# Performance work log

Hardware: AMD Instinct MI355X
Metric: run time of the kernel (lower is better)

## Reference

```python
import jax, jax.numpy as jnp
import numpy as np

D_MODEL = 512
N_HEADS = 8
D_K = D_MODEL // N_HEADS
D_FF = 2048
N = 4096
EPS = 1e-5


def _layer_norm(x, g, b):
    mu = jnp.mean(x, axis=-1, keepdims=True)
    var = jnp.mean(jnp.square(x - mu), axis=-1, keepdims=True)
    return (x - mu) * jax.lax.rsqrt(var + EPS) * g + b


def setup_inputs() -> dict:
    key = jax.random.key(0)
    ks = jax.random.split(key, 16)
    s = 1.0 / np.sqrt(D_MODEL)
    sf = 1.0 / np.sqrt(D_FF)
    inp = {
        "h": jax.random.normal(ks[0], (N, D_MODEL), dtype=jnp.float32),
        "adj": jax.random.randint(ks[1], (N, N), 0, 2, dtype=jnp.int32),
        "Wq": jax.random.uniform(ks[2], (D_MODEL, D_MODEL), jnp.float32, -s, s),
        "bq": jnp.zeros((D_MODEL,), jnp.float32),
        "Wk": jax.random.uniform(ks[3], (D_MODEL, D_MODEL), jnp.float32, -s, s),
        "bk": jnp.zeros((D_MODEL,), jnp.float32),
        "Wv": jax.random.uniform(ks[4], (D_MODEL, D_MODEL), jnp.float32, -s, s),
        "bv": jnp.zeros((D_MODEL,), jnp.float32),
        "Wo": jax.random.uniform(ks[5], (D_MODEL, D_MODEL), jnp.float32, -s, s),
        "bo": jnp.zeros((D_MODEL,), jnp.float32),
        "W1": jax.random.uniform(ks[6], (D_FF, D_MODEL), jnp.float32, -s, s),
        "b1": jnp.zeros((D_FF,), jnp.float32),
        "W2": jax.random.uniform(ks[7], (D_MODEL, D_FF), jnp.float32, -sf, sf),
        "b2": jnp.zeros((D_MODEL,), jnp.float32),
        "ln1_g": jnp.ones((D_MODEL,), jnp.float32),
        "ln1_b": jnp.zeros((D_MODEL,), jnp.float32),
        "ln2_g": jnp.ones((D_MODEL,), jnp.float32),
        "ln2_b": jnp.zeros((D_MODEL,), jnp.float32),
    }
    return inp


def reference(h, adj, Wq, bq, Wk, bk, Wv, bv, Wo, bo, W1, b1, W2, b2,
              ln1_g, ln1_b, ln2_g, ln2_b):
    n = h.shape[0]
    # adjacency + self loops, used as attention mask (batch=1)
    mask = adj.astype(jnp.float32) + jnp.eye(n, dtype=jnp.float32)  # [N,N]

    # QKV projections, split into heads: [N, H, Dk]
    q = (h @ Wq.T + bq).reshape(n, N_HEADS, D_K)
    k = (h @ Wk.T + bk).reshape(n, N_HEADS, D_K)
    v = (h @ Wv.T + bv).reshape(n, N_HEADS, D_K)

    scores = jnp.einsum("nhd,mhd->hnm", q, k) / jnp.sqrt(jnp.float32(D_K))
    scores = jnp.where(mask[None, :, :] == 0, jnp.float32(-1e9), scores)
    attn = jax.nn.softmax(scores, axis=-1)  # dropout is identity in eval
    ctx = jnp.einsum("hnm,mhd->nhd", attn, v).reshape(n, D_MODEL)
    attn_out = ctx @ Wo.T + bo

    h1 = _layer_norm(h + attn_out, ln1_g, ln1_b)
    ff = jax.nn.relu(h1 @ W1.T + b1) @ W2.T + b2
    h2 = _layer_norm(h1 + ff, ln2_g, ln2_b)
    return h2
```

## Files before the change

### kernel.cpp

```cpp
#include <hip/hip_runtime.h>
#include <stdint.h>
#include <stddef.h>

typedef __bf16 bf16;
typedef __bf16 bf16x8 __attribute__((ext_vector_type(8)));
typedef float  f32x4  __attribute__((ext_vector_type(4)));

struct CastArgs {
  const float* src[17];
  bf16*        dst[17];
  int          cum[18];
};

__global__ __launch_bounds__(256) void k_cast(CastArgs a, int total8)
{
  const int g = blockIdx.x * 256 + threadIdx.x;
  if (g >= total8) return;
  int t = 0;
  while (a.cum[t + 1] <= g) ++t;
  const int i = g - a.cum[t];
  const float4* s = (const float4*)(a.src[t]) + (size_t)i * 2;
  const float4 x0 = s[0], x1 = s[1];
  bf16x8 y;
  y[0] = (bf16)x0.x; y[1] = (bf16)x0.y; y[2] = (bf16)x0.z; y[3] = (bf16)x0.w;
  y[4] = (bf16)x1.x; y[5] = (bf16)x1.y; y[6] = (bf16)x1.z; y[7] = (bf16)x1.w;
  *(bf16x8*)(a.dst[t] + (size_t)i * 8) = y;
}

__device__ __forceinline__ void gemm_tile_128(
    const bf16* __restrict__ A, const bf16* __restrict__ B,
    const bf16* __restrict__ bias, bf16* __restrict__ C,
    int N, int K, int m0, int n0, int relu)
{
  __shared__ __align__(16) bf16 As[128 * 72];
  __shared__ __align__(16) bf16 Bs[128 * 72];

  const int tid    = threadIdx.x;
  const int lane   = tid & 63;
  const int wave   = tid >> 6;
  const int lane15 = lane & 15;
  const int quad   = lane >> 4;
  const int wm     = (wave & 1) << 6;
  const int wn     = (wave >> 1) << 6;

  f32x4 acc[4][4] = {};

  const bf16* Ab = A + (size_t)m0 * K;
  const bf16* Bb = B + (size_t)n0 * K;

  for (int k0 = 0; k0 < K; k0 += 64) {
    bf16x8 ar[4], br[4];
#pragma unroll
    for (int i = 0; i < 4; ++i) {
      const int c = i * 256 + tid;
      const int row = c >> 3, col = (c & 7) * 8;
      ar[i] = *(const bf16x8*)&Ab[(size_t)row * K + k0 + col];
      br[i] = *(const bf16x8*)&Bb[(size_t)row * K + k0 + col];
    }
    __syncthreads();
#pragma unroll
    for (int i = 0; i < 4; ++i) {
      const int c = i * 256 + tid;
      const int row = c >> 3, col = c & 7;
      *(bf16x8*)&As[row * 72 + col * 8] = ar[i];
      *(bf16x8*)&Bs[row * 72 + col * 8] = br[i];
    }
    __syncthreads();

#pragma unroll
    for (int kk = 0; kk < 2; ++kk) {
      bf16x8 af[4], bfr[4];
#pragma unroll
      for (int f = 0; f < 4; ++f) {
        const int ra = wm + f * 16 + lane15;
        af[f]  = *(const bf16x8*)&As[ra * 72 + (kk * 4 + quad) * 8];
        const int rb = wn + f * 16 + lane15;
        bfr[f] = *(const bf16x8*)&Bs[rb * 72 + (kk * 4 + quad) * 8];
      }
#pragma unroll
      for (int fm = 0; fm < 4; ++fm)
#pragma unroll
        for (int fn = 0; fn < 4; ++fn)
          acc[fm][fn] = __builtin_amdgcn_mfma_f32_16x16x32_bf16(
              af[fm], bfr[fn], acc[fm][fn], 0, 0, 0);
    }
  }

#pragma unroll
  for (int fm = 0; fm < 4; ++fm) {
#pragma unroll
    for (int fn = 0; fn < 4; ++fn) {
      const int col = n0 + wn + fn * 16 + lane15;
      const float bv = (float)bias[col];
#pragma unroll
      for (int r = 0; r < 4; ++r) {
        const int row = m0 + wm + fm * 16 + quad * 4 + r;
        float v = acc[fm][fn][r] + bv;
        if (relu) v = fmaxf(v, 0.0f);
        C[(size_t)row * N + col] = (bf16)v;
      }
    }
  }
}

__global__ __launch_bounds__(256, 2) void k_gemm(
    const bf16* __restrict__ A, const bf16* __restrict__ B,
    const bf16* __restrict__ bias, bf16* __restrict__ C,
    int N, int K, int relu)
{
  gemm_tile_128(A, B, bias, C, N, K, blockIdx.x * 128, blockIdx.y * 128, relu);
}

__global__ __launch_bounds__(256, 2) void k_gemm_qkv(
    const bf16* __restrict__ h,
    const bf16* __restrict__ Wq, const bf16* __restrict__ Wk, const bf16* __restrict__ Wv,
    const bf16* __restrict__ bq, const bf16* __restrict__ bk, const bf16* __restrict__ bv,
    bf16* __restrict__ q, bf16* __restrict__ k, bf16* __restrict__ v,
    int N, int K)
{
  const bf16* B; const bf16* bias; bf16* C;
  if (blockIdx.z == 0)      { B = Wq; bias = bq; C = q; }
  else if (blockIdx.z == 1) { B = Wk; bias = bk; C = k; }
  else                      { B = Wv; bias = bv; C = v; }
  gemm_tile_128(h, B, bias, C, N, K, blockIdx.x * 128, blockIdx.y * 128, 0);
}

__global__ __launch_bounds__(256, 2) void k_gemm_sk(
    const bf16* __restrict__ A, const bf16* __restrict__ B,
    float* __restrict__ Cp, int N, int K, int Ksplit)
{
  __shared__ __align__(16) bf16 As[128 * 72];
  __shared__ __align__(16) bf16 Bs[128 * 72];

  const int tid    = threadIdx.x;
  const int lane   = tid & 63;
  const int wave   = tid >> 6;
  const int lane15 = lane & 15;
  const int quad   = lane >> 4;
  const int wm     = (wave & 1) << 6;
  const int wn     = (wave >> 1) << 6;
  const int m0     = blockIdx.x * 128;
  const int n0     = blockIdx.y * 128;
  const int kbeg   = blockIdx.z * Ksplit;

  f32x4 acc[4][4] = {};

  const bf16* Ab = A + (size_t)m0 * K;
  const bf16* Bb = B + (size_t)n0 * K;

  for (int k0 = kbeg; k0 < kbeg + Ksplit; k0 += 64) {
    bf16x8 ar[4], br[4];
#pragma unroll
    for (int i = 0; i < 4; ++i) {
      const int c = i * 256 + tid;
      const int row = c >> 3, col = (c & 7) * 8;
      ar[i] = *(const bf16x8*)&Ab[(size_t)row * K + k0 + col];
      br[i] = *(const bf16x8*)&Bb[(size_t)row * K + k0 + col];
    }
    __syncthreads();
#pragma unroll
    for (int i = 0; i < 4; ++i) {
      const int c = i * 256 + tid;
      const int row = c >> 3, col = c & 7;
      *(bf16x8*)&As[row * 72 + col * 8] = ar[i];
      *(bf16x8*)&Bs[row * 72 + col * 8] = br[i];
    }
    __syncthreads();

#pragma unroll
    for (int kk = 0; kk < 2; ++kk) {
      bf16x8 af[4], bfr[4];
#pragma unroll
      for (int f = 0; f < 4; ++f) {
        const int ra = wm + f * 16 + lane15;
        af[f]  = *(const bf16x8*)&As[ra * 72 + (kk * 4 + quad) * 8];
        const int rb = wn + f * 16 + lane15;
        bfr[f] = *(const bf16x8*)&Bs[rb * 72 + (kk * 4 + quad) * 8];
      }
#pragma unroll
      for (int fm = 0; fm < 4; ++fm)
#pragma unroll
        for (int fn = 0; fn < 4; ++fn)
          acc[fm][fn] = __builtin_amdgcn_mfma_f32_16x16x32_bf16(
              af[fm], bfr[fn], acc[fm][fn], 0, 0, 0);
    }
  }

  float* Cz = Cp + (size_t)blockIdx.z * 4096 * N;
#pragma unroll
  for (int fm = 0; fm < 4; ++fm)
#pragma unroll
    for (int fn = 0; fn < 4; ++fn) {
      const int col = n0 + wn + fn * 16 + lane15;
#pragma unroll
      for (int r = 0; r < 4; ++r) {
        const int row = m0 + wm + fm * 16 + quad * 4 + r;
        Cz[(size_t)row * N + col] = acc[fm][fn][r];
      }
    }
}

__global__ __launch_bounds__(256) void k_sk_combine(
    const float* __restrict__ Cp, const bf16* __restrict__ bias,
    bf16* __restrict__ C, int N)
{
  const int g = blockIdx.x * 256 + threadIdx.x;
  const size_t base = (size_t)g * 8;
  const int col = (int)(base % (size_t)N);
  const float* p0 = Cp + base;
  const float* p1 = Cp + (size_t)4096 * N + base;
  f32x4 a0 = *(const f32x4*)p0, a1 = *(const f32x4*)(p0 + 4);
  f32x4 b0 = *(const f32x4*)p1, b1 = *(const f32x4*)(p1 + 4);
  bf16x8 y;
#pragma unroll
  for (int j = 0; j < 4; ++j) {
    y[j]     = (bf16)(a0[j] + b0[j] + (float)bias[col + j]);
    y[4 + j] = (bf16)(a1[j] + b1[j] + (float)bias[col + 4 + j]);
  }
  *(bf16x8*)(C + base) = y;
}

__global__ __launch_bounds__(256) void k_packmask(
    const int* __restrict__ adj, unsigned long long* __restrict__ mb)
{
  const int gw   = (int)((blockIdx.x * 256 + threadIdx.x) >> 6);
  const int lane = threadIdx.x & 63;
  const int a    = adj[(size_t)gw * 64 + lane];
  unsigned long long m = __ballot(a != 0);
  const int row = gw >> 6, wc = gw & 63;
  if ((row >> 6) == wc) m |= 1ull << (row & 63);
  if (lane == 0) mb[gw] = m;
}

__global__ __launch_bounds__(256) void k_transpose_v(
    const bf16* __restrict__ v, bf16* __restrict__ vt)
{
  __shared__ __align__(16) bf16 T[64 * 72];
  const int r0 = blockIdx.x * 64;
  const int c0 = blockIdx.y * 64;
  const int tid = threadIdx.x;
#pragma unroll
  for (int rr = 0; rr < 2; ++rr) {
    int idx = rr * 256 + tid;
    int kr = idx >> 3, ch = (idx & 7) * 8;
    *(bf16x8*)&T[kr * 72 + ch] = *(const bf16x8*)&v[(size_t)(r0 + kr) * 512 + c0 + ch];
  }
  __syncthreads();
#pragma unroll
  for (int rr = 0; rr < 2; ++rr) {
    int idx = rr * 256 + tid;
    int cr = idx >> 3, ch = idx & 7;
    bf16x8 y;
#pragma unroll
    for (int j = 0; j < 8; ++j) y[j] = T[(ch * 8 + j) * 72 + cr];
    *(bf16x8*)&vt[(size_t)(c0 + cr) * 4096 + r0 + ch * 8] = y;
  }
}

__global__ __launch_bounds__(256, 4) void k_attn(
    const bf16* __restrict__ Q, const bf16* __restrict__ Km,
    const bf16* __restrict__ Vt, const unsigned long long* __restrict__ mb,
    bf16* __restrict__ Opart, float* __restrict__ Lpart)
{
  __shared__ __align__(16) bf16 Ks[64 * 72];
  __shared__ __align__(16) bf16 Vs[64 * 72];
  __shared__ __align__(16) bf16 Plb[4][16 * 72];

  const int tid    = threadIdx.x;
  const int wave   = tid >> 6;
  const int lane   = tid & 63;
  const int lane15 = lane & 15;
  const int quad   = lane >> 4;
  const int sp     = blockIdx.x & 3;
  const int hd     = (blockIdx.x >> 2) & 7;
  const int qt     = blockIdx.x >> 5;
  const int qrow   = qt * 64 + wave * 16;

  bf16x8 qf[2];
#pragma unroll
  for (int c = 0; c < 2; ++c)
    qf[c] = *(const bf16x8*)&Q[(size_t)(qrow + lane15) * 512 + hd * 64 + c * 32 + quad * 8];

  bf16x8 ones;
#pragma unroll
  for (int j = 0; j < 8; ++j) ones[j] = (bf16)1.0f;

  f32x4 o[4] = {};
  f32x4 la   = {};

  for (int kt = sp * 16; kt < sp * 16 + 16; ++kt) {
    const int kb = kt * 64;
#pragma unroll
    for (int rr = 0; rr < 2; ++rr) {
      int idx = rr * 256 + tid;
      int a = idx >> 3, ch = (idx & 7) * 8;
      *(bf16x8*)&Ks[a * 72 + ch] = *(const bf16x8*)&Km[(size_t)(kb + a) * 512 + hd * 64 + ch];
      *(bf16x8*)&Vs[a * 72 + ch] = *(const bf16x8*)&Vt[(size_t)(hd * 64 + a) * 4096 + kb + ch];
    }
    __syncthreads();

    unsigned long long mw[4];
#pragma unroll
    for (int r = 0; r < 4; ++r)
      mw[r] = mb[(size_t)(qrow + quad * 4 + r) * 64 + kt] >> lane15;

#pragma unroll
    for (int g = 0; g < 4; ++g) {
      bf16x8 k0f = *(const bf16x8*)&Ks[(g * 16 + lane15) * 72 + quad * 8];
      bf16x8 k1f = *(const bf16x8*)&Ks[(g * 16 + lane15) * 72 + 32 + quad * 8];
      f32x4 s = {};
      s = __builtin_amdgcn_mfma_f32_16x16x32_bf16(qf[0], k0f, s, 0, 0, 0);
      s = __builtin_amdgcn_mfma_f32_16x16x32_bf16(qf[1], k1f, s, 0, 0, 0);
#pragma unroll
      for (int r = 0; r < 4; ++r) {
        const bool ok = ((mw[r] >> (g * 16)) & 1ull) != 0;
        const float p = ok ? __expf(s[r] * 0.125f) : 0.0f;
        Plb[wave][(quad * 4 + r) * 72 + g * 16 + lane15] = (bf16)p;
      }
    }

#pragma unroll
    for (int c2 = 0; c2 < 2; ++c2) {
      bf16x8 pa = *(const bf16x8*)&Plb[wave][lane15 * 72 + c2 * 32 + quad * 8];
      la = __builtin_amdgcn_mfma_f32_16x16x32_bf16(pa, ones, la, 0, 0, 0);
#pragma unroll
      for (int g2 = 0; g2 < 4; ++g2) {
        bf16x8 vf = *(const bf16x8*)&Vs[(g2 * 16 + lane15) * 72 + c2 * 32 + quad * 8];
        o[g2] = __builtin_amdgcn_mfma_f32_16x16x32_bf16(pa, vf, o[g2], 0, 0, 0);
      }
    }
    __syncthreads();
  }

  bf16* Oz = Opart + (size_t)sp * 4096 * 512;
#pragma unroll
  for (int g2 = 0; g2 < 4; ++g2)
#pragma unroll
    for (int r = 0; r < 4; ++r) {
      const int row = qrow + quad * 4 + r;
      Oz[(size_t)row * 512 + hd * 64 + g2 * 16 + lane15] = (bf16)o[g2][r];
    }
  if (lane15 == 0) {
#pragma unroll
    for (int r = 0; r < 4; ++r)
      Lpart[sp * 32768 + (qrow + quad * 4 + r) * 8 + hd] = la[r];
  }
}

__global__ __launch_bounds__(256) void k_attn_combine(
    const bf16* __restrict__ Opart, const float* __restrict__ Lpart,
    bf16* __restrict__ ctx)
{
  const int g = blockIdx.x * 256 + threadIdx.x;
  const size_t base = (size_t)g * 8;
  const int row = g >> 6;
  const int hd  = (g & 63) >> 3;
  float acc[8] = {};
  float l = 0.0f;
#pragma unroll
  for (int s = 0; s < 4; ++s) {
    bf16x8 ov = *(const bf16x8*)&Opart[(size_t)s * 4096 * 512 + base];
#pragma unroll
    for (int j = 0; j < 8; ++j) acc[j] += (float)ov[j];
    l += Lpart[s * 32768 + row * 8 + hd];
  }
  const float rl = 1.0f / l;
  bf16x8 y;
#pragma unroll
  for (int j = 0; j < 8; ++j) y[j] = (bf16)(acc[j] * rl);
  *(bf16x8*)(ctx + base) = y;
}

template <int F32OUT>
__global__ __launch_bounds__(256) void k_addln(
    const bf16* __restrict__ x, const bf16* __restrict__ y,
    const bf16* __restrict__ gam, const bf16* __restrict__ bet,
    void* __restrict__ out)
{
  const int wave = threadIdx.x >> 6, lane = threadIdx.x & 63;
  const int row  = blockIdx.x * 4 + wave;
  const size_t base = (size_t)row * 512 + lane * 8;
  bf16x8 xv = *(const bf16x8*)(x + base);
  bf16x8 yv = *(const bf16x8*)(y + base);
  float v[8], s = 0.0f, s2 = 0.0f;
#pragma unroll
  for (int j = 0; j < 8; ++j) {
    v[j] = (float)xv[j] + (float)yv[j];
    s += v[j]; s2 += v[j] * v[j];
  }
#pragma unroll
  for (int d = 1; d < 64; d <<= 1) { s += __shfl_xor(s, d, 64); s2 += __shfl_xor(s2, d, 64); }
  const float mu  = s * (1.0f / 512.0f);
  const float var = s2 * (1.0f / 512.0f) - mu * mu;
  const float rs  = rsqrtf(var + 1e-5f);
  bf16x8 gv = *(const bf16x8*)(gam + lane * 8);
  bf16x8 bv = *(const bf16x8*)(bet + lane * 8);
  if (F32OUT) {
    float* o = (float*)out + base;
#pragma unroll
    for (int j = 0; j < 8; ++j)
      o[j] = ((v[j] - mu) * rs) * (float)gv[j] + (float)bv[j];
  } else {
    bf16x8 ov;
#pragma unroll
    for (int j = 0; j < 8; ++j)
      ov[j] = (bf16)(((v[j] - mu) * rs) * (float)gv[j] + (float)bv[j]);
    *(bf16x8*)((bf16*)out + base) = ov;
  }
}

extern "C" void kernel_launch(void* const* d_in, const int* in_sizes, int n_in,
                              void* d_out, int out_size, void* d_ws, size_t ws_size,
                              hipStream_t stream)
{
  const int* adj = (const int*)d_in[1];

  char* ws = (char*)d_ws;
  const size_t MB = 1024 * 1024;

  bf16* hb  = (bf16*)(ws + 0 * MB);
  bf16* Wqb = (bf16*)(ws + 4 * MB);
  bf16* Wkb = (bf16*)(ws + 4 * MB + 512 * 1024);
  bf16* Wvb = (bf16*)(ws + 5 * MB);
  bf16* Wob = (bf16*)(ws + 5 * MB + 512 * 1024);
  bf16* W1b = (bf16*)(ws + 6 * MB);
  bf16* W2b = (bf16*)(ws + 8 * MB);
  char* vecbase = ws + 10 * MB;
  bf16* bqb  = (bf16*)(vecbase + 0 * 16384);
  bf16* bkb  = (bf16*)(vecbase + 1 * 16384);
  bf16* bvb  = (bf16*)(vecbase + 2 * 16384);
  bf16* bob  = (bf16*)(vecbase + 3 * 16384);
  bf16* b1b  = (bf16*)(vecbase + 4 * 16384);
  bf16* b2b  = (bf16*)(vecbase + 5 * 16384);
  bf16* g1b  = (bf16*)(vecbase + 6 * 16384);
  bf16* be1b = (bf16*)(vecbase + 7 * 16384);
  bf16* g2b  = (bf16*)(vecbase + 8 * 16384);
  bf16* be2b = (bf16*)(vecbase + 9 * 16384);

  bf16* q    = (bf16*)(ws + 12 * MB);
  bf16* k    = (bf16*)(ws + 16 * MB);
  bf16* v    = (bf16*)(ws + 20 * MB);
  bf16* vt   = (bf16*)(ws + 24 * MB);
  unsigned long long* mbits = (unsigned long long*)(ws + 28 * MB);
  bf16* ctx  = (bf16*)(ws + 30 * MB);
  bf16*  Opart = (bf16*)(ws + 34 * MB);
  float* Lpart = (float*)(ws + 50 * MB);
  float* skP  = (float*)(ws + 34 * MB);
  bf16* att  = (bf16*)(ws + 12 * MB);
  bf16* h1   = (bf16*)(ws + 30 * MB);
  bf16* ff1  = (bf16*)(ws + 12 * MB);
  bf16* ff2  = (bf16*)(ws + 12 * MB);

  CastArgs ca;
  const int srcIdx[17] = {0, 2, 3, 4, 5, 6, 7, 8, 9, 10, 11, 12, 13, 14, 15, 16, 17};
  bf16* dsts[17] = {hb, Wqb, bqb, Wkb, bkb, Wvb, bvb, Wob, bob,
                    W1b, b1b, W2b, b2b, g1b, be1b, g2b, be2b};
  int cum = 0;
  for (int t = 0; t < 17; ++t) {
    ca.src[t] = (const float*)d_in[srcIdx[t]];
    ca.dst[t] = dsts[t];
    ca.cum[t] = cum;
    cum += in_sizes[srcIdx[t]] / 8;
  }
  ca.cum[17] = cum;

  const dim3 blk(256);
  k_cast<<<dim3((cum + 255) / 256), blk, 0, stream>>>(ca, cum);

  k_gemm_qkv<<<dim3(32, 4, 3), blk, 0, stream>>>(hb, Wqb, Wkb, Wvb, bqb, bkb, bvb,
                                                 q, k, v, 512, 512);
  k_transpose_v<<<dim3(64, 8), blk, 0, stream>>>(v, vt);
  k_packmask<<<dim3(65536), blk, 0, stream>>>(adj, mbits);
  k_attn<<<dim3(2048), blk, 0, stream>>>(q, k, vt, mbits, Opart, Lpart);
  k_attn_combine<<<dim3(1024), blk, 0, stream>>>(Opart, Lpart, ctx);
  k_gemm_sk<<<dim3(32, 4, 2), blk, 0, stream>>>(ctx, Wob, skP, 512, 512, 256);
  k_sk_combine<<<dim3(1024), blk, 0, stream>>>(skP, bob, att, 512);
  k_addln<0><<<dim3(1024), blk, 0, stream>>>(hb, att, g1b, be1b, (void*)h1);
  k_gemm<<<dim3(32, 16), blk, 0, stream>>>(h1, W1b, b1b, ff1, 2048, 512, 1);
  k_gemm_sk<<<dim3(32, 4, 2), blk, 0, stream>>>(ff1, W2b, skP, 512, 2048, 1024);
  k_sk_combine<<<dim3(1024), blk, 0, stream>>>(skP, b2b, ff2, 512);
  k_addln<1><<<dim3(1024), blk, 0, stream>>>(h1, ff2, g2b, be2b, d_out);
}
```

Baseline: 322.3 us.

## Async LDS GEMM loads, fuse split-K combine into LayerNorm, widen attention tiles

GEMM tiles now use global_load_lds async copies into an XOR-swizzled unpadded LDS layout instead of register staging. The split-K combine kernels are folded into the add+LayerNorm kernels, which removes two launches and an intermediate round trip through memory. The attention kernel processes 32 query rows per wave, halving the grid and reusing K/V fragments across two M tiles. Bias and LayerNorm vectors are read directly as fp32, so they no longer go through the cast kernel. The wider attention tiles raise register and LDS pressure, and the async path adds a trailing barrier each k-step.

```diff
diff --git a/kernel.cpp b/kernel.cpp
--- a/kernel.cpp
+++ b/kernel.cpp
@@ -6,10 +6,18 @@
 typedef __bf16 bf16x8 __attribute__((ext_vector_type(8)));
 typedef float  f32x4  __attribute__((ext_vector_type(4)));
 
+typedef __attribute__((address_space(3))) void       lds_void;
+typedef __attribute__((address_space(1))) const void gbl_cvoid;
+
+#define ASYNC_CP16(g, l) \
+  __builtin_amdgcn_global_load_lds((gbl_cvoid*)(g), (lds_void*)(l), 16, 0, 0)
+
+__device__ __forceinline__ int swz(int r) { return (r & 7) ^ ((r & 8) >> 1); }
+
 struct CastArgs {
-  const float* src[17];
-  bf16*        dst[17];
-  int          cum[18];
+  const float* src[7];
+  bf16*        dst[7];
+  int          cum[8];
 };
 
 __global__ __launch_bounds__(256) void k_cast(CastArgs a, int total8)
@@ -27,14 +35,11 @@
   *(bf16x8*)(a.dst[t] + (size_t)i * 8) = y;
 }
 
-__device__ __forceinline__ void gemm_tile_128(
+__device__ __forceinline__ void gemm_core_async(
     const bf16* __restrict__ A, const bf16* __restrict__ B,
-    const bf16* __restrict__ bias, bf16* __restrict__ C,
-    int N, int K, int m0, int n0, int relu)
-{
-  __shared__ __align__(16) bf16 As[128 * 72];
-  __shared__ __align__(16) bf16 Bs[128 * 72];
-
+    bf16* As, bf16* Bs, f32x4 (&acc)[4][4],
+    int K, int m0, int n0, int kbeg, int kend)
+{
   const int tid    = threadIdx.x;
   const int lane   = tid & 63;
   const int wave   = tid >> 6;
@@ -43,27 +48,22 @@
   const int wm     = (wave & 1) << 6;
   const int wn     = (wave >> 1) << 6;
 
-  f32x4 acc[4][4] = {};
+  int srow[4], soff[4];
+#pragma unroll
+  for (int i = 0; i < 4; ++i) {
+    int c   = ((wave * 4 + i) << 6) + lane;
+    srow[i] = c >> 3;
+    soff[i] = ((c & 7) ^ swz(srow[i])) * 8;
+  }
 
   const bf16* Ab = A + (size_t)m0 * K;
   const bf16* Bb = B + (size_t)n0 * K;
 
-  for (int k0 = 0; k0 < K; k0 += 64) {
-    bf16x8 ar[4], br[4];
+  for (int k0 = kbeg; k0 < kend; k0 += 64) {
 #pragma unroll
     for (int i = 0; i < 4; ++i) {
-      const int c = i * 256 + tid;
-      const int row = c >> 3, col = (c & 7) * 8;
-      ar[i] = *(const bf16x8*)&Ab[(size_t)row * K + k0 + col];
-      br[i] = *(const bf16x8*)&Bb[(size_t)row * K + k0 + col];
-    }
-    __syncthreads();
-#pragma unroll
-    for (int i = 0; i < 4; ++i) {
-      const int c = i * 256 + tid;
-      const int row = c >> 3, col = c & 7;
-      *(bf16x8*)&As[row * 72 + col * 8] = ar[i];
-      *(bf16x8*)&Bs[row * 72 + col * 8] = br[i];
+      ASYNC_CP16(Ab + (size_t)srow[i] * K + k0 + soff[i], &As[(wave * 4 + i) * 512]);
+      ASYNC_CP16(Bb + (size_t)srow[i] * K + k0 + soff[i], &Bs[(wave * 4 + i) * 512]);
     }
     __syncthreads();
 
@@ -73,9 +73,9 @@
 #pragma unroll
       for (int f = 0; f < 4; ++f) {
         const int ra = wm + f * 16 + lane15;
-        af[f]  = *(const bf16x8*)&As[ra * 72 + (kk * 4 + quad) * 8];
+        af[f]  = *(const bf16x8*)&As[ra * 64 + (((kk * 4 + quad) ^ swz(ra)) * 8)];
         const int rb = wn + f * 16 + lane15;
-        bfr[f] = *(const bf16x8*)&Bs[rb * 72 + (kk * 4 + quad) * 8];
+        bfr[f] = *(const bf16x8*)&Bs[rb * 64 + (((kk * 4 + quad) ^ swz(rb)) * 8)];
       }
 #pragma unroll
       for (int fm = 0; fm < 4; ++fm)
@@ -84,14 +84,31 @@
           acc[fm][fn] = __builtin_amdgcn_mfma_f32_16x16x32_bf16(
               af[fm], bfr[fn], acc[fm][fn], 0, 0, 0);
     }
-  }
-
-#pragma unroll
-  for (int fm = 0; fm < 4; ++fm) {
+    __syncthreads();
+  }
+}
+
+__global__ __launch_bounds__(256, 2) void k_gemm(
+    const bf16* __restrict__ A, const bf16* __restrict__ B,
+    const float* __restrict__ bias, bf16* __restrict__ C,
+    int N, int K, int relu)
+{
+  __shared__ __align__(16) bf16 As[128 * 64];
+  __shared__ __align__(16) bf16 Bs[128 * 64];
+  const int m0 = blockIdx.x * 128, n0 = blockIdx.y * 128;
+  f32x4 acc[4][4] = {};
+  gemm_core_async(A, B, As, Bs, acc, K, m0, n0, 0, K);
+
+  const int lane15 = threadIdx.x & 15;
+  const int quad   = (threadIdx.x & 63) >> 4;
+  const int wave   = threadIdx.x >> 6;
+  const int wm     = (wave & 1) << 6, wn = (wave >> 1) << 6;
+#pragma unroll
+  for (int fm = 0; fm < 4; ++fm)
 #pragma unroll
     for (int fn = 0; fn < 4; ++fn) {
       const int col = n0 + wn + fn * 16 + lane15;
-      const float bv = (float)bias[col];
+      const float bv = bias[col];
 #pragma unroll
       for (int r = 0; r < 4; ++r) {
         const int row = m0 + wm + fm * 16 + quad * 4 + r;
@@ -100,92 +117,57 @@
         C[(size_t)row * N + col] = (bf16)v;
       }
     }
-  }
-}
-
-__global__ __launch_bounds__(256, 2) void k_gemm(
-    const bf16* __restrict__ A, const bf16* __restrict__ B,
-    const bf16* __restrict__ bias, bf16* __restrict__ C,
-    int N, int K, int relu)
-{
-  gemm_tile_128(A, B, bias, C, N, K, blockIdx.x * 128, blockIdx.y * 128, relu);
 }
 
 __global__ __launch_bounds__(256, 2) void k_gemm_qkv(
     const bf16* __restrict__ h,
     const bf16* __restrict__ Wq, const bf16* __restrict__ Wk, const bf16* __restrict__ Wv,
-    const bf16* __restrict__ bq, const bf16* __restrict__ bk, const bf16* __restrict__ bv,
-    bf16* __restrict__ q, bf16* __restrict__ k, bf16* __restrict__ v,
-    int N, int K)
-{
-  const bf16* B; const bf16* bias; bf16* C;
+    const float* __restrict__ bq, const float* __restrict__ bk, const float* __restrict__ bv,
+    bf16* __restrict__ q, bf16* __restrict__ k, bf16* __restrict__ v)
+{
+  __shared__ __align__(16) bf16 As[128 * 64];
+  __shared__ __align__(16) bf16 Bs[128 * 64];
+  const bf16* B; const float* bias; bf16* C;
   if (blockIdx.z == 0)      { B = Wq; bias = bq; C = q; }
   else if (blockIdx.z == 1) { B = Wk; bias = bk; C = k; }
   else                      { B = Wv; bias = bv; C = v; }
-  gemm_tile_128(h, B, bias, C, N, K, blockIdx.x * 128, blockIdx.y * 128, 0);
+  const int m0 = blockIdx.x * 128, n0 = blockIdx.y * 128;
+  f32x4 acc[4][4] = {};
+  gemm_core_async(h, B, As, Bs, acc, 512, m0, n0, 0, 512);
+
+  const int lane15 = threadIdx.x & 15;
+  const int quad   = (threadIdx.x & 63) >> 4;
+  const int wave   = threadIdx.x >> 6;
+  const int wm     = (wave & 1) << 6, wn = (wave >> 1) << 6;
+#pragma unroll
+  for (int fm = 0; fm < 4; ++fm)
+#pragma unroll
+    for (int fn = 0; fn < 4; ++fn) {
+      const int col = n0 + wn + fn * 16 + lane15;
+      const float bv = bias[col];
+#pragma unroll
+      for (int r = 0; r < 4; ++r) {
+        const int row = m0 + wm + fm * 16 + quad * 4 + r;
+        C[(size_t)row * 512 + col] = (bf16)(acc[fm][fn][r] + bv);
+      }
+    }
 }
 
 __global__ __launch_bounds__(256, 2) void k_gemm_sk(
     const bf16* __restrict__ A, const bf16* __restrict__ B,
     float* __restrict__ Cp, int N, int K, int Ksplit)
 {
-  __shared__ __align__(16) bf16 As[128 * 72];
-  __shared__ __align__(16) bf16 Bs[128 * 72];
-
-  const int tid    = threadIdx.x;
-  const int lane   = tid & 63;
-  const int wave   = tid >> 6;
-  const int lane15 = lane & 15;
-  const int quad   = lane >> 4;
-  const int wm     = (wave & 1) << 6;
-  const int wn     = (wave >> 1) << 6;
-  const int m0     = blockIdx.x * 128;
-  const int n0     = blockIdx.y * 128;
-  const int kbeg   = blockIdx.z * Ksplit;
-
+  __shared__ __align__(16) bf16 As[128 * 64];
+  __shared__ __align__(16) bf16 Bs[128 * 64];
+  const int m0 = blockIdx.x * 128, n0 = blockIdx.y * 128;
+  const int kbeg = blockIdx.z * Ksplit;
   f32x4 acc[4][4] = {};
-
-  const bf16* Ab = A + (size_t)m0 * K;
-  const bf16* Bb = B + (size_t)n0 * K;
-
-  for (int k0 = kbeg; k0 < kbeg + Ksplit; k0 += 64) {
-    bf16x8 ar[4], br[4];
-#pragma unroll
-    for (int i = 0; i < 4; ++i) {
-      const int c = i * 256 + tid;
-      const int row = c >> 3, col = (c & 7) * 8;
-      ar[i] = *(const bf16x8*)&Ab[(size_t)row * K + k0 + col];
-      br[i] = *(const bf16x8*)&Bb[(size_t)row * K + k0 + col];
-    }
-    __syncthreads();
-#pragma unroll
-    for (int i = 0; i < 4; ++i) {
-      const int c = i * 256 + tid;
-      const int row = c >> 3, col = c & 7;
-      *(bf16x8*)&As[row * 72 + col * 8] = ar[i];
-      *(bf16x8*)&Bs[row * 72 + col * 8] = br[i];
-    }
-    __syncthreads();
-
-#pragma unroll
-    for (int kk = 0; kk < 2; ++kk) {
-      bf16x8 af[4], bfr[4];
-#pragma unroll
-      for (int f = 0; f < 4; ++f) {
-        const int ra = wm + f * 16 + lane15;
-        af[f]  = *(const bf16x8*)&As[ra * 72 + (kk * 4 + quad) * 8];
-        const int rb = wn + f * 16 + lane15;
-        bfr[f] = *(const bf16x8*)&Bs[rb * 72 + (kk * 4 + quad) * 8];
-      }
-#pragma unroll
-      for (int fm = 0; fm < 4; ++fm)
-#pragma unroll
-        for (int fn = 0; fn < 4; ++fn)
-          acc[fm][fn] = __builtin_amdgcn_mfma_f32_16x16x32_bf16(
-              af[fm], bfr[fn], acc[fm][fn], 0, 0, 0);
-    }
-  }
-
+  gemm_core_async(A, B, As, Bs, acc, K, m0, n0, kbeg, kbeg + Ksplit);
+
+  const int lane15 = threadIdx.x & 15;
+  const int quad   = (threadIdx.x & 63) >> 4;
+  const int wave   = threadIdx.x >> 6;
+  const int wm     = (wave & 1) << 6, wn = (wave >> 1) << 6;
   float* Cz = Cp + (size_t)blockIdx.z * 4096 * N;
 #pragma unroll
   for (int fm = 0; fm < 4; ++fm)
@@ -198,26 +180,6 @@
         Cz[(size_t)row * N + col] = acc[fm][fn][r];
       }
     }
-}
-
-__global__ __launch_bounds__(256) void k_sk_combine(
-    const float* __restrict__ Cp, const bf16* __restrict__ bias,
-    bf16* __restrict__ C, int N)
-{
-  const int g = blockIdx.x * 256 + threadIdx.x;
-  const size_t base = (size_t)g * 8;
-  const int col = (int)(base % (size_t)N);
-  const float* p0 = Cp + base;
-  const float* p1 = Cp + (size_t)4096 * N + base;
-  f32x4 a0 = *(const f32x4*)p0, a1 = *(const f32x4*)(p0 + 4);
-  f32x4 b0 = *(const f32x4*)p1, b1 = *(const f32x4*)(p1 + 4);
-  bf16x8 y;
-#pragma unroll
-  for (int j = 0; j < 4; ++j) {
-    y[j]     = (bf16)(a0[j] + b0[j] + (float)bias[col + j]);
-    y[4 + j] = (bf16)(a1[j] + b1[j] + (float)bias[col + 4 + j]);
-  }
-  *(bf16x8*)(C + base) = y;
 }
 
 __global__ __launch_bounds__(256) void k_packmask(
@@ -264,7 +226,7 @@
 {
   __shared__ __align__(16) bf16 Ks[64 * 72];
   __shared__ __align__(16) bf16 Vs[64 * 72];
-  __shared__ __align__(16) bf16 Plb[4][16 * 72];
+  __shared__ __align__(16) bf16 Plb[4][32 * 72];
 
   const int tid    = threadIdx.x;
   const int wave   = tid >> 6;
@@ -274,19 +236,22 @@
   const int sp     = blockIdx.x & 3;
   const int hd     = (blockIdx.x >> 2) & 7;
   const int qt     = blockIdx.x >> 5;
-  const int qrow   = qt * 64 + wave * 16;
-
-  bf16x8 qf[2];
-#pragma unroll
-  for (int c = 0; c < 2; ++c)
-    qf[c] = *(const bf16x8*)&Q[(size_t)(qrow + lane15) * 512 + hd * 64 + c * 32 + quad * 8];
+  const int qrow   = qt * 128 + wave * 32;
+
+  bf16x8 qf[2][2];
+#pragma unroll
+  for (int mt = 0; mt < 2; ++mt)
+#pragma unroll
+    for (int c = 0; c < 2; ++c)
+      qf[mt][c] = *(const bf16x8*)&Q[(size_t)(qrow + mt * 16 + lane15) * 512 +
+                                     hd * 64 + c * 32 + quad * 8];
 
   bf16x8 ones;
 #pragma unroll
   for (int j = 0; j < 8; ++j) ones[j] = (bf16)1.0f;
 
-  f32x4 o[4] = {};
-  f32x4 la   = {};
+  f32x4 o[2][4] = {};
+  f32x4 la[2]   = {};
 
   for (int kt = sp * 16; kt < sp * 16 + 16; ++kt) {
     const int kb = kt * 64;
@@ -299,51 +264,64 @@
     }
     __syncthreads();
 
-    unsigned long long mw[4];
-#pragma unroll
-    for (int r = 0; r < 4; ++r)
-      mw[r] = mb[(size_t)(qrow + quad * 4 + r) * 64 + kt] >> lane15;
+    unsigned long long mw[2][4];
+#pragma unroll
+    for (int mt = 0; mt < 2; ++mt)
+#pragma unroll
+      for (int r = 0; r < 4; ++r)
+        mw[mt][r] = mb[(size_t)(qrow + mt * 16 + quad * 4 + r) * 64 + kt] >> lane15;
 
 #pragma unroll
     for (int g = 0; g < 4; ++g) {
       bf16x8 k0f = *(const bf16x8*)&Ks[(g * 16 + lane15) * 72 + quad * 8];
       bf16x8 k1f = *(const bf16x8*)&Ks[(g * 16 + lane15) * 72 + 32 + quad * 8];
-      f32x4 s = {};
-      s = __builtin_amdgcn_mfma_f32_16x16x32_bf16(qf[0], k0f, s, 0, 0, 0);
-      s = __builtin_amdgcn_mfma_f32_16x16x32_bf16(qf[1], k1f, s, 0, 0, 0);
+#pragma unroll
+      for (int mt = 0; mt < 2; ++mt) {
+        f32x4 s = {};
+        s = __builtin_amdgcn_mfma_f32_16x16x32_bf16(qf[mt][0], k0f, s, 0, 0, 0);
+        s = __builtin_amdgcn_mfma_f32_16x16x32_bf16(qf[mt][1], k1f, s, 0, 0, 0);
+#pragma unroll
+        for (int r = 0; r < 4; ++r) {
+          const bool ok = ((mw[mt][r] >> (g * 16)) & 1ull) != 0;
+          const float p = ok ? __expf(s[r] * 0.125f) : 0.0f;
+          Plb[wave][(mt * 16 + quad * 4 + r) * 72 + g * 16 + lane15] = (bf16)p;
+        }
+      }
+    }
+
+#pragma unroll
+    for (int c2 = 0; c2 < 2; ++c2) {
+      bf16x8 vf[4];
+#pragma unroll
+      for (int g2 = 0; g2 < 4; ++g2)
+        vf[g2] = *(const bf16x8*)&Vs[(g2 * 16 + lane15) * 72 + c2 * 32 + quad * 8];
+#pragma unroll
+      for (int mt = 0; mt < 2; ++mt) {
+        bf16x8 pa = *(const bf16x8*)&Plb[wave][(mt * 16 + lane15) * 72 + c2 * 32 + quad * 8];
+        la[mt] = __builtin_amdgcn_mfma_f32_16x16x32_bf16(pa, ones, la[mt], 0, 0, 0);
+#pragma unroll
+        for (int g2 = 0; g2 < 4; ++g2)
+          o[mt][g2] = __builtin_amdgcn_mfma_f32_16x16x32_bf16(pa, vf[g2], o[mt][g2], 0, 0, 0);
+      }
+    }
+    __syncthreads();
+  }
+
+  bf16* Oz = Opart + (size_t)sp * 4096 * 512;
+#pragma unroll
+  for (int mt = 0; mt < 2; ++mt) {
+#pragma unroll
+    for (int g2 = 0; g2 < 4; ++g2)
 #pragma unroll
       for (int r = 0; r < 4; ++r) {
-        const bool ok = ((mw[r] >> (g * 16)) & 1ull) != 0;
-        const float p = ok ? __expf(s[r] * 0.125f) : 0.0f;
-        Plb[wave][(quad * 4 + r) * 72 + g * 16 + lane15] = (bf16)p;
-      }
-    }
-
-#pragma unroll
-    for (int c2 = 0; c2 < 2; ++c2) {
-      bf16x8 pa = *(const bf16x8*)&Plb[wave][lane15 * 72 + c2 * 32 + quad * 8];
-      la = __builtin_amdgcn_mfma_f32_16x16x32_bf16(pa, ones, la, 0, 0, 0);
-#pragma unroll
-      for (int g2 = 0; g2 < 4; ++g2) {
-        bf16x8 vf = *(const bf16x8*)&Vs[(g2 * 16 + lane15) * 72 + c2 * 32 + quad * 8];
-        o[g2] = __builtin_amdgcn_mfma_f32_16x16x32_bf16(pa, vf, o[g2], 0, 0, 0);
-      }
-    }
-    __syncthreads();
-  }
-
-  bf16* Oz = Opart + (size_t)sp * 4096 * 512;
-#pragma unroll
-  for (int g2 = 0; g2 < 4; ++g2)
-#pragma unroll
-    for (int r = 0; r < 4; ++r) {
-      const int row = qrow + quad * 4 + r;
-      Oz[(size_t)row * 512 + hd * 64 + g2 * 16 + lane15] = (bf16)o[g2][r];
-    }
-  if (lane15 == 0) {
-#pragma unroll
-    for (int r = 0; r < 4; ++r)
-      Lpart[sp * 32768 + (qrow + quad * 4 + r) * 8 + hd] = la[r];
+        const int row = qrow + mt * 16 + quad * 4 + r;
+        Oz[(size_t)row * 512 + hd * 64 + g2 * 16 + lane15] = (bf16)o[mt][g2][r];
+      }
+    if (lane15 == 0) {
+#pragma unroll
+      for (int r = 0; r < 4; ++r)
+        Lpart[sp * 32768 + (qrow + mt * 16 + quad * 4 + r) * 8 + hd] = la[mt][r];
+    }
   }
 }
 
@@ -372,39 +350,51 @@
 }
 
 template <int F32OUT>
-__global__ __launch_bounds__(256) void k_addln(
-    const bf16* __restrict__ x, const bf16* __restrict__ y,
-    const bf16* __restrict__ gam, const bf16* __restrict__ bet,
+__global__ __launch_bounds__(256) void k_addln_sk(
+    const bf16* __restrict__ x, const float* __restrict__ Cp,
+    const float* __restrict__ bias,
+    const float* __restrict__ gam, const float* __restrict__ bet,
     void* __restrict__ out)
 {
   const int wave = threadIdx.x >> 6, lane = threadIdx.x & 63;
   const int row  = blockIdx.x * 4 + wave;
   const size_t base = (size_t)row * 512 + lane * 8;
+  const int col = lane * 8;
   bf16x8 xv = *(const bf16x8*)(x + base);
-  bf16x8 yv = *(const bf16x8*)(y + base);
+  const float* p0 = Cp + base;
+  const float* p1 = Cp + (size_t)4096 * 512 + base;
+  f32x4 a0 = *(const f32x4*)p0, a1 = *(const f32x4*)(p0 + 4);
+  f32x4 b0 = *(const f32x4*)p1, b1 = *(const f32x4*)(p1 + 4);
+  f32x4 c0 = *(const f32x4*)(bias + col), c1 = *(const f32x4*)(bias + col + 4);
   float v[8], s = 0.0f, s2 = 0.0f;
 #pragma unroll
-  for (int j = 0; j < 8; ++j) {
-    v[j] = (float)xv[j] + (float)yv[j];
-    s += v[j]; s2 += v[j] * v[j];
-  }
+  for (int j = 0; j < 4; ++j) {
+    v[j]     = (float)xv[j]     + a0[j] + b0[j] + c0[j];
+    v[4 + j] = (float)xv[4 + j] + a1[j] + b1[j] + c1[j];
+  }
+#pragma unroll
+  for (int j = 0; j < 8; ++j) { s += v[j]; s2 += v[j] * v[j]; }
 #pragma unroll
   for (int d = 1; d < 64; d <<= 1) { s += __shfl_xor(s, d, 64); s2 += __shfl_xor(s2, d, 64); }
   const float mu  = s * (1.0f / 512.0f);
   const float var = s2 * (1.0f / 512.0f) - mu * mu;
   const float rs  = rsqrtf(var + 1e-5f);
-  bf16x8 gv = *(const bf16x8*)(gam + lane * 8);
-  bf16x8 bv = *(const bf16x8*)(bet + lane * 8);
+  f32x4 g0 = *(const f32x4*)(gam + col), g1 = *(const f32x4*)(gam + col + 4);
+  f32x4 e0 = *(const f32x4*)(bet + col), e1 = *(const f32x4*)(bet + col + 4);
   if (F32OUT) {
     float* o = (float*)out + base;
 #pragma unroll
-    for (int j = 0; j < 8; ++j)
-      o[j] = ((v[j] - mu) * rs) * (float)gv[j] + (float)bv[j];
+    for (int j = 0; j < 4; ++j) {
+      o[j]     = ((v[j] - mu) * rs) * g0[j] + e0[j];
+      o[4 + j] = ((v[4 + j] - mu) * rs) * g1[j] + e1[j];
+    }
   } else {
     bf16x8 ov;
 #pragma unroll
-    for (int j = 0; j < 8; ++j)
-      ov[j] = (bf16)(((v[j] - mu) * rs) * (float)gv[j] + (float)bv[j]);
+    for (int j = 0; j < 4; ++j) {
+      ov[j]     = (bf16)(((v[j] - mu) * rs) * g0[j] + e0[j]);
+      ov[4 + j] = (bf16)(((v[4 + j] - mu) * rs) * g1[j] + e1[j]);
+    }
     *(bf16x8*)((bf16*)out + base) = ov;
   }
 }
@@ -413,7 +403,17 @@
                               void* d_out, int out_size, void* d_ws, size_t ws_size,
                               hipStream_t stream)
 {
-  const int* adj = (const int*)d_in[1];
+  const int*   adj = (const int*)  d_in[1];
+  const float* bq  = (const float*)d_in[3];
+  const float* bk  = (const float*)d_in[5];
+  const float* bv  = (const float*)d_in[7];
+  const float* bo  = (const float*)d_in[9];
+  const float* b1  = (const float*)d_in[11];
+  const float* b2  = (const float*)d_in[13];
+  const float* g1  = (const float*)d_in[14];
+  const float* be1 = (const float*)d_in[15];
+  const float* g2  = (const float*)d_in[16];
+  const float* be2 = (const float*)d_in[17];
 
   char* ws = (char*)d_ws;
   const size_t MB = 1024 * 1024;
@@ -425,17 +425,6 @@
   bf16* Wob = (bf16*)(ws + 5 * MB + 512 * 1024);
   bf16* W1b = (bf16*)(ws + 6 * MB);
   bf16* W2b = (bf16*)(ws + 8 * MB);
-  char* vecbase = ws + 10 * MB;
-  bf16* bqb  = (bf16*)(vecbase + 0 * 16384);
-  bf16* bkb  = (bf16*)(vecbase + 1 * 16384);
-  bf16* bvb  = (bf16*)(vecbase + 2 * 16384);
-  bf16* bob  = (bf16*)(vecbase + 3 * 16384);
-  bf16* b1b  = (bf16*)(vecbase + 4 * 16384);
-  bf16* b2b  = (bf16*)(vecbase + 5 * 16384);
-  bf16* g1b  = (bf16*)(vecbase + 6 * 16384);
-  bf16* be1b = (bf16*)(vecbase + 7 * 16384);
-  bf16* g2b  = (bf16*)(vecbase + 8 * 16384);
-  bf16* be2b = (bf16*)(vecbase + 9 * 16384);
 
   bf16* q    = (bf16*)(ws + 12 * MB);
   bf16* k    = (bf16*)(ws + 16 * MB);
@@ -445,39 +434,33 @@
   bf16* ctx  = (bf16*)(ws + 30 * MB);
   bf16*  Opart = (bf16*)(ws + 34 * MB);
   float* Lpart = (float*)(ws + 50 * MB);
-  float* skP  = (float*)(ws + 34 * MB);
-  bf16* att  = (bf16*)(ws + 12 * MB);
-  bf16* h1   = (bf16*)(ws + 30 * MB);
-  bf16* ff1  = (bf16*)(ws + 12 * MB);
-  bf16* ff2  = (bf16*)(ws + 12 * MB);
+  float* skP   = (float*)(ws + 34 * MB);
+  bf16* h1   = (bf16*)(ws + 12 * MB);
+  bf16* ff1  = (bf16*)(ws + 16 * MB);
 
   CastArgs ca;
-  const int srcIdx[17] = {0, 2, 3, 4, 5, 6, 7, 8, 9, 10, 11, 12, 13, 14, 15, 16, 17};
-  bf16* dsts[17] = {hb, Wqb, bqb, Wkb, bkb, Wvb, bvb, Wob, bob,
-                    W1b, b1b, W2b, b2b, g1b, be1b, g2b, be2b};
+  const int srcIdx[7] = {0, 2, 4, 6, 8, 10, 12};
+  bf16* dsts[7] = {hb, Wqb, Wkb, Wvb, Wob, W1b, W2b};
   int cum = 0;
-  for (int t = 0; t < 17; ++t) {
+  for (int t = 0; t < 7; ++t) {
     ca.src[t] = (const float*)d_in[srcIdx[t]];
     ca.dst[t] = dsts[t];
     ca.cum[t] = cum;
     cum += in_sizes[srcIdx[t]] / 8;
   }
-  ca.cum[17] = cum;
+  ca.cum[7] = cum;
 
   const dim3 blk(256);
   k_cast<<<dim3((cum + 255) / 256), blk, 0, stream>>>(ca, cum);
 
-  k_gemm_qkv<<<dim3(32, 4, 3), blk, 0, stream>>>(hb, Wqb, Wkb, Wvb, bqb, bkb, bvb,
-                                                 q, k, v, 512, 512);
+  k_gemm_qkv<<<dim3(32, 4, 3), blk, 0, stream>>>(hb, Wqb, Wkb, Wvb, bq, bk, bv, q, k, v);
   k_transpose_v<<<dim3(64, 8), blk, 0, stream>>>(v, vt);
   k_packmask<<<dim3(65536), blk, 0, stream>>>(adj, mbits);
-  k_attn<<<dim3(2048), blk, 0, stream>>>(q, k, vt, mbits, Opart, Lpart);
+  k_attn<<<dim3(1024), blk, 0, stream>>>(q, k, vt, mbits, Opart, Lpart);
   k_attn_combine<<<dim3(1024), blk, 0, stream>>>(Opart, Lpart, ctx);
   k_gemm_sk<<<dim3(32, 4, 2), blk, 0, stream>>>(ctx, Wob, skP, 512, 512, 256);
-  k_sk_combine<<<dim3(1024), blk, 0, stream>>>(skP, bob, att, 512);
-  k_addln<0><<<dim3(1024), blk, 0, stream>>>(hb, att, g1b, be1b, (void*)h1);
-  k_gemm<<<dim3(32, 16), blk, 0, stream>>>(h1, W1b, b1b, ff1, 2048, 512, 1);
+  k_addln_sk<0><<<dim3(1024), blk, 0, stream>>>(hb, skP, bo, g1, be1, (void*)h1);
+  k_gemm<<<dim3(32, 16), blk, 0, stream>>>(h1, W1b, b1, ff1, 2048, 512, 1);
   k_gemm_sk<<<dim3(32, 4, 2), blk, 0, stream>>>(ff1, W2b, skP, 512, 2048, 1024);
-  k_sk_combine<<<dim3(1024), blk, 0, stream>>>(skP, b2b, ff2, 512);
-  k_addln<1><<<dim3(1024), blk, 0, stream>>>(h1, ff2, g2b, be2b, d_out);
-}
+  k_addln_sk<1><<<dim3(1024), blk, 0, stream>>>(h1, skP, b2, g2, be2, d_out);
+}
```

Result: faster. 311.8 us (-3.2%).
